# Kernel tuning notes

Measured on AMD Instinct MI355X. Metric: run time of the kernel, lower is better.

The kernel has to match this reference:

```python
import jax, jax.numpy as jnp
import numpy as np

KERNEL_SIZE = 9  # spatial kernel extent used only for output cropping


def setup_inputs() -> dict:
    key = jax.random.key(0)
    k1, k2, k3, k4 = jax.random.split(key, 4)
    B, Cin, Cout, H, W = 32, 64, 128, 128, 128
    Wf = W // 2 + 1  # rfft bins on last dim (W even, no pad branch)
    return {
        "signal": jax.random.normal(k1, (B, Cin, H, W), dtype=jnp.float32),
        "weight_real": jax.random.normal(k2, (Cout, Cin, H, Wf), dtype=jnp.float32),
        "weight_imag": jax.random.normal(k3, (Cout, Cin, H, Wf), dtype=jnp.float32),
        "bias": jax.random.normal(k4, (Cout,), dtype=jnp.float32),
    }


def reference(signal, weight_real, weight_imag, bias):
    # FFT conv with a frequency-domain complex kernel (groups=1, padding=0,
    # stride=1). Matches torch fft_conv: rfftn -> complex matmul over channels
    # per frequency bin -> irfftn -> crop -> bias add.
    B, Cin, H, W = signal.shape
    sig_fr = jnp.fft.rfftn(signal, axes=(2, 3))            # [B, Cin, H, W//2+1] c64
    kernel = (weight_real + 1j * weight_imag).astype(jnp.complex64)
    # complex_matmul with groups=1: contract Cin per (h,w) frequency bin
    out_fr = jnp.einsum('bihw,oihw->bohw', sig_fr, kernel)  # [B, Cout, H, W//2+1]
    out = jnp.fft.irfftn(out_fr, axes=(2, 3))               # [B, Cout, H, W] real
    Ho = H - KERNEL_SIZE + 1
    Wo = W - KERNEL_SIZE + 1
    out = out[:, :, :Ho, :Wo]
    out = out + bias[None, :, None, None]
    return out
```

## Files before the change

### kernel.cpp

```cpp
#include <hip/hip_runtime.h>
#include <math.h>

#define DI __device__ __forceinline__

constexpr int Hh   = 128;
constexpr int Ww   = 128;
constexpr int WF   = 65;
constexpr int NBIN = Hh * WF;
constexpr int NB   = 32;
constexpr int CIN  = 64;
constexpr int COUT = 128;
constexpr int HO   = 120;
constexpr int WO   = 120;

typedef __bf16 bf16x8 __attribute__((ext_vector_type(8)));
typedef float  f32x16 __attribute__((ext_vector_type(16)));

DI unsigned int bfbits(float x) {
  unsigned int u = __float_as_uint(x);
  return (u + 0x7FFFu + ((u >> 16) & 1u)) >> 16;
}
DI unsigned int packbf(float re, float im) { return bfbits(re) | (bfbits(im) << 16); }
DI float2 unpackbf(unsigned int v) {
  return make_float2(__uint_as_float(v << 16), __uint_as_float(v & 0xFFFF0000u));
}

DI f32x16 MFMA32(uint4 a, uint4 b, f32x16 c) {
  return __builtin_amdgcn_mfma_f32_32x32x16_bf16(
      __builtin_bit_cast(bf16x8, a), __builtin_bit_cast(bf16x8, b), c, 0, 0, 0);
}
DI unsigned int rotneg(unsigned int x) { return ((x << 16) | (x >> 16)) ^ 0x80000000u; }
DI uint4 derive(uint4 s) {
  uint4 r; r.x = rotneg(s.x); r.y = rotneg(s.y); r.z = rotneg(s.z); r.w = rotneg(s.w);
  return r;
}

DI int bitrev6(int l) {
  return ((l & 1) << 5) | ((l & 2) << 3) | ((l & 4) << 1) |
         ((l & 8) >> 1) | ((l & 16) >> 3) | ((l & 32) >> 5);
}
DI float2 cmul(float2 a, float2 b) {
  return make_float2(a.x * b.x - a.y * b.y, a.x * b.y + a.y * b.x);
}
DI float2 sxor(float2 v, int m) {
  return make_float2(__shfl_xor(v.x, m), __shfl_xor(v.y, m));
}
DI float bpermf(int addr, float v) {
  return __int_as_float(__builtin_amdgcn_ds_bpermute(addr, __float_as_int(v)));
}
DI void stg(float2& v, int h, float2 tw, int l) {
  float2 p = sxor(v, h);
  float2 s = make_float2(v.x + p.x, v.y + p.y);
  float2 d = make_float2(p.x - v.x, p.y - v.y);
  float2 m = cmul(d, tw);
  v = (l & h) ? m : s;
}
DI void stg1(float2& v, int l) {
  float2 p = sxor(v, 1);
  v = (l & 1) ? make_float2(p.x - v.x, p.y - v.y)
              : make_float2(v.x + p.x, v.y + p.y);
}
DI void twinit(float2* tw, int l) {
  float s_, c_;
  __sincosf(-(float)M_PI * (float)l / 64.f, &s_, &c_);
  tw[0] = make_float2(c_, s_);
#pragma unroll
  for (int i = 0; i < 5; ++i) {
    const int h = 32 >> i;
    __sincosf(-(float)M_PI * (float)(l & (h - 1)) / (float)h, &s_, &c_);
    tw[1 + i] = make_float2(c_, s_);
  }
}
DI void sfft128x2(float2& a0, float2& b0, float2& a1, float2& b1,
                  const float2* tw, int l) {
  {
    float2 s = make_float2(a0.x + b0.x, a0.y + b0.y);
    float2 d = make_float2(a0.x - b0.x, a0.y - b0.y);
    a0 = s; b0 = cmul(d, tw[0]);
  }
  {
    float2 s = make_float2(a1.x + b1.x, a1.y + b1.y);
    float2 d = make_float2(a1.x - b1.x, a1.y - b1.y);
    a1 = s; b1 = cmul(d, tw[0]);
  }
#pragma unroll
  for (int i = 0; i < 5; ++i) {
    const int h = 32 >> i;
    stg(a0, h, tw[1 + i], l); stg(a1, h, tw[1 + i], l);
    stg(b0, h, tw[1 + i], l); stg(b1, h, tw[1 + i], l);
  }
  stg1(a0, l); stg1(a1, l); stg1(b0, l); stg1(b1, l);
}

__global__ __launch_bounds__(256) void fwd_fft(const float* __restrict__ sig,
                                               unsigned int* __restrict__ sf) {
  __shared__ unsigned int sImg[NBIN];

  const int t = threadIdx.x, grp = t >> 6, l = t & 63;
  const size_t img = blockIdx.x;
  const float* src = sig + img * (size_t)(Hh * Ww);
  unsigned int* dst = sf + img * (size_t)NBIN;

  float2 tw[6]; twinit(tw, l);
  const int br = bitrev6(l);
  const int sk4 = bitrev6(l >> 1) * 4;
  const int im  = (128 - l) & 127;
  const int sm4 = bitrev6(im >> 1) * 4;
  const bool podd = (l & 1) != 0;

  for (int batch = 0; batch < 8; ++batch) {
    float2 a[2], b[2];
#pragma unroll
    for (int f = 0; f < 2; ++f) {
      const int jp = batch * 8 + grp * 2 + f;
      const float* r0 = src + (size_t)(2 * jp) * Ww;
      a[f] = make_float2(r0[l],      r0[Ww + l]);
      b[f] = make_float2(r0[64 + l], r0[Ww + 64 + l]);
    }
    sfft128x2(a[0], b[0], a[1], b[1], tw, l);
#pragma unroll
    for (int f = 0; f < 2; ++f) {
      const int jp = batch * 8 + grp * 2 + f;
      float axk = bpermf(sk4, a[f].x), ayk = bpermf(sk4, a[f].y);
      float bxk = bpermf(sk4, b[f].x), byk = bpermf(sk4, b[f].y);
      float axm = bpermf(sm4, a[f].x), aym = bpermf(sm4, a[f].y);
      float bxm = bpermf(sm4, b[f].x), bym = bpermf(sm4, b[f].y);
      float z64x = bpermf(4, a[f].x),  z64y = bpermf(4, a[f].y);
      float2 Zk = podd ? make_float2(bxk, byk) : make_float2(axk, ayk);
      float2 Zm = podd ? make_float2(bxm, bym) : make_float2(axm, aym);
      sImg[(2 * jp) * WF + l]     = packbf(0.5f * (Zk.x + Zm.x), 0.5f * (Zk.y - Zm.y));
      sImg[(2 * jp + 1) * WF + l] = packbf(0.5f * (Zk.y + Zm.y), 0.5f * (Zm.x - Zk.x));
      if (l == 0) {
        sImg[(2 * jp) * WF + 64]     = packbf(z64x, 0.f);
        sImg[(2 * jp + 1) * WF + 64] = packbf(z64y, 0.f);
      }
    }
  }
  __syncthreads();

  for (int batch = 0; batch < 9; ++batch) {
    float2 a[2], b[2]; int wcol[2];
#pragma unroll
    for (int f = 0; f < 2; ++f) {
      const int w = batch * 8 + grp * 2 + f; wcol[f] = w;
      const int wc = (w < WF) ? w : (WF - 1);
      a[f] = unpackbf(sImg[l * WF + wc]);
      b[f] = unpackbf(sImg[(l + 64) * WF + wc]);
    }
    sfft128x2(a[0], b[0], a[1], b[1], tw, l);
#pragma unroll
    for (int f = 0; f < 2; ++f) {
      if (wcol[f] < WF) {
        sImg[(2 * br) * WF + wcol[f]]     = packbf(a[f].x, a[f].y);
        sImg[(2 * br + 1) * WF + wcol[f]] = packbf(b[f].x, b[f].y);
      }
    }
  }
  __syncthreads();

  const uint4* s4 = (const uint4*)sImg;
  uint4* d4 = (uint4*)dst;
  for (int idx = t; idx < NBIN / 4; idx += 256) d4[idx] = s4[idx];
}

constexpr int PT    = 16;
constexpr int PLANE = 260;

__global__ __launch_bounds__(512, 4) void spec_mm(const unsigned int* __restrict__ sf,
                                                  const float* __restrict__ wr,
                                                  const float* __restrict__ wi,
                                                  unsigned int* __restrict__ of) {
  __shared__ unsigned int wbuf[PT * PLANE];
  __shared__ unsigned int sbuf[PT * PLANE];

  const int t = threadIdx.x;
  const int bid = blockIdx.x;
  const int swz = (bid & 7) * 260 + (bid >> 3);
  const int o0 = (swz & 3) * 32;
  const int p0 = (swz >> 2) * PT;

  const int po = t & 3;
  const int ii = (t >> 2) & 7;
  const int rl = (t >> 5) & 15;

  const float* wrp0 = wr + ((size_t)(o0 + rl) * CIN + ii) * NBIN + p0 + po * 4;
  const float* wip0 = wi + ((size_t)(o0 + rl) * CIN + ii) * NBIN + p0 + po * 4;
  const unsigned int* sfp0 = sf + ((size_t)rl * CIN + ii) * NBIN + p0 + po * 4;
  const size_t rowAdv = (size_t)16 * CIN * NBIN;

  auto slotOf = [](int row, int i) {
    return ((((row * 2) + (i >> 2)) ^ ((row >> 2) & 7)) << 2) + (i & 3);
  };
  const int slotLo = slotOf(rl, ii);
  const int slotHi = slotOf(rl + 16, ii);

  const int l = t & 63, wv = t >> 6;
  const int lr = l & 31, lq = l >> 5;
  const int moff = ((((lr * 2) + lq) ^ ((lr >> 2) & 7)) << 2);
  const int pA = 2 * wv, pB = 2 * wv + 1;

  f32x16 aR0 = {}, aI0 = {}, aR1 = {}, aI1 = {};

  float4 w0r, w1r, w0i, w1i; uint4 s0v, s1v;
  {
    w0r = *(const float4*)(wrp0);          w1r = *(const float4*)(wrp0 + rowAdv);
    w0i = *(const float4*)(wip0);          w1i = *(const float4*)(wip0 + rowAdv);
    s0v = *(const uint4*)(sfp0);           s1v = *(const uint4*)(sfp0 + rowAdv);
  }

  for (int kq = 0; kq < 8; ++kq) {
    const float* a0 = (const float*)&w0r;  const float* a1 = (const float*)&w1r;
    const float* b0 = (const float*)&w0i;  const float* b1 = (const float*)&w1i;
    const unsigned int* u0 = (const unsigned int*)&s0v;
    const unsigned int* u1 = (const unsigned int*)&s1v;
#pragma unroll
    for (int j = 0; j < 4; ++j) {
      const int pp = (po * 4 + j) * PLANE;
      wbuf[pp + slotLo] = packbf(a0[j], -b0[j]);
      wbuf[pp + slotHi] = packbf(a1[j], -b1[j]);
      sbuf[pp + slotLo] = u0[j];
      sbuf[pp + slotHi] = u1[j];
    }
    if (kq < 7) {
      const size_t adv = (size_t)(kq + 1) * 8 * NBIN;
      w0r = *(const float4*)(wrp0 + adv);  w1r = *(const float4*)(wrp0 + adv + rowAdv);
      w0i = *(const float4*)(wip0 + adv);  w1i = *(const float4*)(wip0 + adv + rowAdv);
      s0v = *(const uint4*)(sfp0 + adv);   s1v = *(const uint4*)(sfp0 + adv + rowAdv);
    }
    __syncthreads();

    {
      const uint4 a = *(const uint4*)&wbuf[pA * PLANE + moff];
      const uint4 s = *(const uint4*)&sbuf[pA * PLANE + moff];
      aR0 = MFMA32(a, s, aR0);
      aI0 = MFMA32(a, derive(s), aI0);
    }
    {
      const uint4 a = *(const uint4*)&wbuf[pB * PLANE + moff];
      const uint4 s = *(const uint4*)&sbuf[pB * PLANE + moff];
      aR1 = MFMA32(a, s, aR1);
      aI1 = MFMA32(a, derive(s), aI1);
    }
    __syncthreads();
  }

  const int b = lr;
#pragma unroll
  for (int r = 0; r < 16; ++r) {
    const int o = o0 + (r & 3) + 8 * (r >> 2) + 4 * lq;
    uint2 v;
    v.x = packbf(aR0[r], aI0[r]);
    v.y = packbf(aR1[r], aI1[r]);
    *(uint2*)(of + ((size_t)b * COUT + o) * NBIN + p0 + 2 * wv) = v;
  }
}

__global__ __launch_bounds__(256) void inv_fft(const unsigned int* __restrict__ of,
                                               const float* __restrict__ bias,
                                               float* __restrict__ out) {
  __shared__ unsigned int sImg[NBIN];

  const int t = threadIdx.x, grp = t >> 6, l = t & 63;
  const size_t img = blockIdx.x;
  const unsigned int* src = of + img * (size_t)NBIN;
  float* dst = out + img * (size_t)(HO * WO);
  const float bo = bias[img & (COUT - 1)];

  float2 tw[6]; twinit(tw, l);
  const int br = bitrev6(l);

  const uint4* s4 = (const uint4*)src;
  uint4* d4 = (uint4*)sImg;
  for (int idx = t; idx < NBIN / 4; idx += 256) d4[idx] = s4[idx];
  __syncthreads();

  for (int batch = 0; batch < 9; ++batch) {
    float2 a[2], b[2]; int wcol[2];
#pragma unroll
    for (int f = 0; f < 2; ++f) {
      const int w = batch * 8 + grp * 2 + f; wcol[f] = w;
      const int wc = (w < WF) ? w : (WF - 1);
      float2 za = unpackbf(sImg[l * WF + wc]);
      float2 zb = unpackbf(sImg[(l + 64) * WF + wc]);
      a[f] = make_float2(za.x, -za.y);
      b[f] = make_float2(zb.x, -zb.y);
    }
    sfft128x2(a[0], b[0], a[1], b[1], tw, l);
#pragma unroll
    for (int f = 0; f < 2; ++f) {
      if (wcol[f] < WF) {
        sImg[(2 * br) * WF + wcol[f]]     = packbf(a[f].x, -a[f].y);
        sImg[(2 * br + 1) * WF + wcol[f]] = packbf(b[f].x, -b[f].y);
      }
    }
  }
  __syncthreads();

  const float sc = 1.f / 16384.f;
  for (int batch = 0; batch < 8; ++batch) {
    float2 a[2], b[2]; int jpv[2];
#pragma unroll
    for (int f = 0; f < 2; ++f) {
      const int jp = batch * 8 + grp * 2 + f; jpv[f] = jp;
      const int jc = (jp < 60) ? jp : 59;
      const unsigned int* X0p = &sImg[(size_t)(2 * jc) * WF];
      const unsigned int* X1p = X0p + WF;
      float2 za, zb;
      if (l == 0) {
        za = make_float2(unpackbf(X0p[0]).x,  unpackbf(X1p[0]).x);
        zb = make_float2(unpackbf(X0p[64]).x, unpackbf(X1p[64]).x);
      } else {
        float2 x0 = unpackbf(X0p[l]), x1 = unpackbf(X1p[l]);
        za = make_float2(x0.x - x1.y, x0.y + x1.x);
        const int mI = 64 - l;
        float2 y0 = unpackbf(X0p[mI]), y1 = unpackbf(X1p[mI]);
        zb = make_float2(y0.x + y1.y, y1.x - y0.y);
      }
      a[f] = make_float2(za.x, -za.y);
      b[f] = make_float2(zb.x, -zb.y);
    }
    sfft128x2(a[0], b[0], a[1], b[1], tw, l);
    const int n0 = 2 * br;
#pragma unroll
    for (int f = 0; f < 2; ++f) {
      const int jp = jpv[f];
      if (jp < 60 && n0 < WO) {
        float2 r0 = make_float2(a[f].x * sc + bo,  b[f].x * sc + bo);
        float2 r1 = make_float2(-a[f].y * sc + bo, -b[f].y * sc + bo);
        *(float2*)(dst + (size_t)(2 * jp) * WO + n0)     = r0;
        *(float2*)(dst + (size_t)(2 * jp + 1) * WO + n0) = r1;
      }
    }
  }
}

extern "C" void kernel_launch(void* const* d_in, const int* in_sizes, int n_in,
                              void* d_out, int out_size, void* d_ws, size_t ws_size,
                              hipStream_t stream) {
  const float* signal = (const float*)d_in[0];
  const float* wr     = (const float*)d_in[1];
  const float* wi     = (const float*)d_in[2];
  const float* bias   = (const float*)d_in[3];
  float* out = (float*)d_out;

  unsigned int* sig_fr = (unsigned int*)d_out;
  unsigned int* out_fr = (unsigned int*)d_ws;
  (void)in_sizes; (void)n_in; (void)out_size; (void)ws_size;

  fwd_fft<<<NB * CIN, 256, 0, stream>>>(signal, sig_fr);
  spec_mm<<<2080, 512, 0, stream>>>(sig_fr, wr, wi, out_fr);
  inv_fft<<<NB * COUT, 256, 0, stream>>>(out_fr, bias, out);
}
```

Baseline: 489.8 us.

## Load spectral matmul operands directly into registers, removing LDS staging and barriers

```diff
diff --git a/kernel.cpp b/kernel.cpp
--- a/kernel.cpp
+++ b/kernel.cpp
@@ -163,95 +163,70 @@
   for (int idx = t; idx < NBIN / 4; idx += 256) d4[idx] = s4[idx];
 }
 
-constexpr int PT    = 16;
-constexpr int PLANE = 260;
-
-__global__ __launch_bounds__(512, 4) void spec_mm(const unsigned int* __restrict__ sf,
+__global__ __launch_bounds__(256, 4) void spec_mm(const unsigned int* __restrict__ sf,
                                                   const float* __restrict__ wr,
                                                   const float* __restrict__ wi,
                                                   unsigned int* __restrict__ of) {
-  __shared__ unsigned int wbuf[PT * PLANE];
-  __shared__ unsigned int sbuf[PT * PLANE];
-
   const int t = threadIdx.x;
-  const int bid = blockIdx.x;
-  const int swz = (bid & 7) * 260 + (bid >> 3);
-  const int o0 = (swz & 3) * 32;
-  const int p0 = (swz >> 2) * PT;
-
-  const int po = t & 3;
-  const int ii = (t >> 2) & 7;
-  const int rl = (t >> 5) & 15;
-
-  const float* wrp0 = wr + ((size_t)(o0 + rl) * CIN + ii) * NBIN + p0 + po * 4;
-  const float* wip0 = wi + ((size_t)(o0 + rl) * CIN + ii) * NBIN + p0 + po * 4;
-  const unsigned int* sfp0 = sf + ((size_t)rl * CIN + ii) * NBIN + p0 + po * 4;
-  const size_t rowAdv = (size_t)16 * CIN * NBIN;
-
-  auto slotOf = [](int row, int i) {
-    return ((((row * 2) + (i >> 2)) ^ ((row >> 2) & 7)) << 2) + (i & 3);
-  };
-  const int slotLo = slotOf(rl, ii);
-  const int slotHi = slotOf(rl + 16, ii);
-
   const int l = t & 63, wv = t >> 6;
   const int lr = l & 31, lq = l >> 5;
-  const int moff = ((((lr * 2) + lq) ^ ((lr >> 2) & 7)) << 2);
-  const int pA = 2 * wv, pB = 2 * wv + 1;
+
+  const int bid = blockIdx.x;
+  const int swzb = (bid & 7) * 520 + (bid >> 3);
+  const int tid = swzb * 4 + wv;
+  const int otile = tid / 4160;
+  const int pp = tid - otile * 4160;
+  const int o0 = otile * 32;
+  const int p0 = pp * 2;
+
+  const float* wrp = wr + ((size_t)(o0 + lr) * CIN + lq * 4) * NBIN + p0;
+  const float* wip = wi + ((size_t)(o0 + lr) * CIN + lq * 4) * NBIN + p0;
+  const unsigned int* sfp = sf + ((size_t)lr * CIN + lq * 4) * NBIN + p0;
 
   f32x16 aR0 = {}, aI0 = {}, aR1 = {}, aI1 = {};
 
-  float4 w0r, w1r, w0i, w1i; uint4 s0v, s1v;
-  {
-    w0r = *(const float4*)(wrp0);          w1r = *(const float4*)(wrp0 + rowAdv);
-    w0i = *(const float4*)(wip0);          w1i = *(const float4*)(wip0 + rowAdv);
-    s0v = *(const uint4*)(sfp0);           s1v = *(const uint4*)(sfp0 + rowAdv);
-  }
-
-  for (int kq = 0; kq < 8; ++kq) {
-    const float* a0 = (const float*)&w0r;  const float* a1 = (const float*)&w1r;
-    const float* b0 = (const float*)&w0i;  const float* b1 = (const float*)&w1i;
-    const unsigned int* u0 = (const unsigned int*)&s0v;
-    const unsigned int* u1 = (const unsigned int*)&s1v;
+  float2 wrA[4], wiA[4]; uint2 svA[4];
+  float2 wrB[4], wiB[4]; uint2 svB[4];
+
+  auto LOAD = [&](float2* w_, float2* i_, uint2* s_, int kq) {
+    const size_t ib = (size_t)kq * 8 * NBIN;
 #pragma unroll
     for (int j = 0; j < 4; ++j) {
-      const int pp = (po * 4 + j) * PLANE;
-      wbuf[pp + slotLo] = packbf(a0[j], -b0[j]);
-      wbuf[pp + slotHi] = packbf(a1[j], -b1[j]);
-      sbuf[pp + slotLo] = u0[j];
-      sbuf[pp + slotHi] = u1[j];
-    }
-    if (kq < 7) {
-      const size_t adv = (size_t)(kq + 1) * 8 * NBIN;
-      w0r = *(const float4*)(wrp0 + adv);  w1r = *(const float4*)(wrp0 + adv + rowAdv);
-      w0i = *(const float4*)(wip0 + adv);  w1i = *(const float4*)(wip0 + adv + rowAdv);
-      s0v = *(const uint4*)(sfp0 + adv);   s1v = *(const uint4*)(sfp0 + adv + rowAdv);
-    }
-    __syncthreads();
-
-    {
-      const uint4 a = *(const uint4*)&wbuf[pA * PLANE + moff];
-      const uint4 s = *(const uint4*)&sbuf[pA * PLANE + moff];
-      aR0 = MFMA32(a, s, aR0);
-      aI0 = MFMA32(a, derive(s), aI0);
-    }
-    {
-      const uint4 a = *(const uint4*)&wbuf[pB * PLANE + moff];
-      const uint4 s = *(const uint4*)&sbuf[pB * PLANE + moff];
-      aR1 = MFMA32(a, s, aR1);
-      aI1 = MFMA32(a, derive(s), aI1);
-    }
-    __syncthreads();
-  }
-
-  const int b = lr;
+      const size_t a = ib + (size_t)j * NBIN;
+      w_[j] = *(const float2*)(wrp + a);
+      i_[j] = *(const float2*)(wip + a);
+      s_[j] = *(const uint2*)(sfp + a);
+    }
+  };
+  auto COMPUTE = [&](const float2* w_, const float2* i_, const uint2* s_) {
+    uint4 a0, a1, s0, s1;
+    a0.x = packbf(w_[0].x, -i_[0].x); a0.y = packbf(w_[1].x, -i_[1].x);
+    a0.z = packbf(w_[2].x, -i_[2].x); a0.w = packbf(w_[3].x, -i_[3].x);
+    a1.x = packbf(w_[0].y, -i_[0].y); a1.y = packbf(w_[1].y, -i_[1].y);
+    a1.z = packbf(w_[2].y, -i_[2].y); a1.w = packbf(w_[3].y, -i_[3].y);
+    s0.x = s_[0].x; s0.y = s_[1].x; s0.z = s_[2].x; s0.w = s_[3].x;
+    s1.x = s_[0].y; s1.y = s_[1].y; s1.z = s_[2].y; s1.w = s_[3].y;
+    aR0 = MFMA32(a0, s0, aR0); aI0 = MFMA32(a0, derive(s0), aI0);
+    aR1 = MFMA32(a1, s1, aR1); aI1 = MFMA32(a1, derive(s1), aI1);
+  };
+
+  LOAD(wrA, wiA, svA, 0);
+  LOAD(wrB, wiB, svB, 1);
+#pragma unroll
+  for (int k2 = 0; k2 < 4; ++k2) {
+    COMPUTE(wrA, wiA, svA);
+    if (k2 < 3) LOAD(wrA, wiA, svA, 2 * k2 + 2);
+    COMPUTE(wrB, wiB, svB);
+    if (k2 < 3) LOAD(wrB, wiB, svB, 2 * k2 + 3);
+  }
+
 #pragma unroll
   for (int r = 0; r < 16; ++r) {
     const int o = o0 + (r & 3) + 8 * (r >> 2) + 4 * lq;
     uint2 v;
     v.x = packbf(aR0[r], aI0[r]);
     v.y = packbf(aR1[r], aI1[r]);
-    *(uint2*)(of + ((size_t)b * COUT + o) * NBIN + p0 + 2 * wv) = v;
+    *(uint2*)(of + ((size_t)lr * COUT + o) * NBIN + p0) = v;
   }
 }
 
@@ -348,6 +323,6 @@
   (void)in_sizes; (void)n_in; (void)out_size; (void)ws_size;
 
   fwd_fft<<<NB * CIN, 256, 0, stream>>>(signal, sig_fr);
-  spec_mm<<<2080, 512, 0, stream>>>(sig_fr, wr, wi, out_fr);
+  spec_mm<<<4160, 256, 0, stream>>>(sig_fr, wr, wi, out_fr);
   inv_fft<<<NB * COUT, 256, 0, stream>>>(out_fr, bias, out);
 }
```

Result: slower. 709.5 us (+44.8%).
